# Performance work log

Measured on AMD Instinct MI355X. Metric: run time of the kernel, lower is better.

The kernel has to match this reference:

```python
import jax, jax.numpy as jnp
import numpy as np


def setup_inputs() -> dict:
    key = jax.random.key(0)
    ks = jax.random.split(key, 6)
    B, V, C, T = 32, 2048, 64, 64
    x = jax.random.normal(ks[0], (B, V, C, T), dtype=jnp.float32)
    U_1 = jax.random.normal(ks[1], (V,), dtype=jnp.float32)
    U_2 = jax.random.normal(ks[2], (C, V), dtype=jnp.float32)
    U_3 = jax.random.normal(ks[3], (C,), dtype=jnp.float32)
    b_e = jax.random.normal(ks[4], (1, T, T), dtype=jnp.float32)
    V_e = jax.random.normal(ks[5], (B, T, T), dtype=jnp.float32)
    return {"x": x, "U_1": U_1, "U_2": U_2, "U_3": U_3, "b_e": b_e, "V_e": V_e}


def reference(x, U_1, U_2, U_3, b_e, V_e):
    # x: (B, V, C, T)
    # lhs = (x^T . U_1) . U_2  -> (B, T, V)
    lhs = jnp.einsum('bvct,v->btc', x, U_1) @ U_2          # (B,T,C) @ (C,V) -> (B,T,V)
    # rhs = x^T . U_3 -> (B, V, T)
    rhs = jnp.einsum('bvct,c->bvt', x, U_3)                # (B,V,T)
    product = jnp.einsum('btv,bvu->btu', lhs, rhs)          # (B,T,T)
    # E = V_e @ sigmoid(product + b_e); V_e broadcast over batch
    E = jnp.einsum('bts,bsu->btu', V_e, jax.nn.sigmoid(product + b_e))  # (B,T,T)
    # manual softmax along dim 1 (shift-invariant -> equivalent to jax.nn.softmax)
    return jax.nn.softmax(E, axis=1)
```

## Files before the change

### kernel.cpp

```cpp
#include <hip/hip_runtime.h>
#include <math.h>

#define NB 32
#define NV 2048
#define NC 64
#define NT 64
#define VC 128
#define CHUNKS (NV / VC)
#define U2P 68

__global__ __launch_bounds__(256) void k1_pass_x(
    const float* __restrict__ x,
    const float* __restrict__ U1,
    const float* __restrict__ U2,
    const float* __restrict__ U3,
    float* __restrict__ part)
{
    const int tid = threadIdx.x;
    const int blk = blockIdx.x;
    const int b     = blk / CHUNKS;
    const int chunk = blk % CHUNKS;
    const int v0    = chunk * VC;

    const int w    = tid >> 6;
    const int l    = tid & 63;
    const int u0   = (l & 15) * 4;
    const int crow = l >> 4;
    const int cw   = w * 16 + crow;

    __shared__ float U2s[VC][U2P];
    __shared__ float Msum[NC * NT];

    for (int i = tid; i < VC * NC; i += 256) {
        const int c  = i >> 7;
        const int vi = i & 127;
        U2s[vi][c] = U2[c * NV + v0 + vi];
    }

    float u3r[4];
#pragma unroll
    for (int k = 0; k < 4; ++k) u3r[k] = U3[cw + 4 * k];

    float4 t1r[4], mr[16];
#pragma unroll
    for (int k = 0; k < 4; ++k) t1r[k] = make_float4(0.f, 0.f, 0.f, 0.f);
#pragma unroll
    for (int j = 0; j < 16; ++j) mr[j] = make_float4(0.f, 0.f, 0.f, 0.f);

    __syncthreads();

    const float* xb = x + (size_t)(b * NV + v0) * (NC * NT) + cw * NT + u0;

    float4 xc[4];
#pragma unroll
    for (int k = 0; k < 4; ++k)
        xc[k] = *reinterpret_cast<const float4*>(xb + 4 * k * NT);

#pragma unroll 2
    for (int vi = 0; vi < VC; ++vi) {
        const int vn = (vi + 1 < VC) ? vi + 1 : vi;
        const float* xv = xb + (size_t)vn * (NC * NT);
        float4 xn[4];
#pragma unroll
        for (int k = 0; k < 4; ++k)
            xn[k] = *reinterpret_cast<const float4*>(xv + 4 * k * NT);

        const float u1v = U1[v0 + vi];

        float4 rh = make_float4(0.f, 0.f, 0.f, 0.f);
#pragma unroll
        for (int k = 0; k < 4; ++k) {
            t1r[k].x = fmaf(u1v, xc[k].x, t1r[k].x);
            t1r[k].y = fmaf(u1v, xc[k].y, t1r[k].y);
            t1r[k].z = fmaf(u1v, xc[k].z, t1r[k].z);
            t1r[k].w = fmaf(u1v, xc[k].w, t1r[k].w);
            rh.x = fmaf(u3r[k], xc[k].x, rh.x);
            rh.y = fmaf(u3r[k], xc[k].y, rh.y);
            rh.z = fmaf(u3r[k], xc[k].z, rh.z);
            rh.w = fmaf(u3r[k], xc[k].w, rh.w);
        }

#pragma unroll
        for (int m = 16; m <= 32; m <<= 1) {
            rh.x += __shfl_xor(rh.x, m, 64);
            rh.y += __shfl_xor(rh.y, m, 64);
            rh.z += __shfl_xor(rh.z, m, 64);
            rh.w += __shfl_xor(rh.w, m, 64);
        }

#pragma unroll
        for (int j4 = 0; j4 < 4; ++j4) {
            const float4 u2v = *reinterpret_cast<const float4*>(
                &U2s[vi][crow * 16 + 4 * j4]);
            mr[4 * j4 + 0].x = fmaf(u2v.x, rh.x, mr[4 * j4 + 0].x);
            mr[4 * j4 + 0].y = fmaf(u2v.x, rh.y, mr[4 * j4 + 0].y);
            mr[4 * j4 + 0].z = fmaf(u2v.x, rh.z, mr[4 * j4 + 0].z);
            mr[4 * j4 + 0].w = fmaf(u2v.x, rh.w, mr[4 * j4 + 0].w);
            mr[4 * j4 + 1].x = fmaf(u2v.y, rh.x, mr[4 * j4 + 1].x);
            mr[4 * j4 + 1].y = fmaf(u2v.y, rh.y, mr[4 * j4 + 1].y);
            mr[4 * j4 + 1].z = fmaf(u2v.y, rh.z, mr[4 * j4 + 1].z);
            mr[4 * j4 + 1].w = fmaf(u2v.y, rh.w, mr[4 * j4 + 1].w);
            mr[4 * j4 + 2].x = fmaf(u2v.z, rh.x, mr[4 * j4 + 2].x);
            mr[4 * j4 + 2].y = fmaf(u2v.z, rh.y, mr[4 * j4 + 2].y);
            mr[4 * j4 + 2].z = fmaf(u2v.z, rh.z, mr[4 * j4 + 2].z);
            mr[4 * j4 + 2].w = fmaf(u2v.z, rh.w, mr[4 * j4 + 2].w);
            mr[4 * j4 + 3].x = fmaf(u2v.w, rh.x, mr[4 * j4 + 3].x);
            mr[4 * j4 + 3].y = fmaf(u2v.w, rh.y, mr[4 * j4 + 3].y);
            mr[4 * j4 + 3].z = fmaf(u2v.w, rh.z, mr[4 * j4 + 3].z);
            mr[4 * j4 + 3].w = fmaf(u2v.w, rh.w, mr[4 * j4 + 3].w);
        }

#pragma unroll
        for (int k = 0; k < 4; ++k) xc[k] = xn[k];
    }

    float* pb = part + (size_t)(b * CHUNKS + chunk) * 2 * NC * NT;

#pragma unroll
    for (int k = 0; k < 4; ++k)
        *reinterpret_cast<float4*>(&pb[(cw + 4 * k) * NT + u0]) = t1r[k];

    for (int i = 0; i < 4; ++i) {
        if (w == i) {
#pragma unroll
            for (int j = 0; j < 16; ++j) {
                float* d = &Msum[(crow * 16 + j) * NT + u0];
                if (i == 0) {
                    *reinterpret_cast<float4*>(d) = mr[j];
                } else {
                    d[0] += mr[j].x; d[1] += mr[j].y;
                    d[2] += mr[j].z; d[3] += mr[j].w;
                }
            }
        }
        __syncthreads();
    }

    float* pbM = pb + NC * NT;
    for (int i = tid * 4; i < NC * NT; i += 1024)
        *reinterpret_cast<float4*>(&pbM[i]) =
            *reinterpret_cast<const float4*>(&Msum[i]);
}

__global__ __launch_bounds__(256) void k2a_reduce(
    const float4* __restrict__ part4,
    float4* __restrict__ fin4)
{
    const int j = blockIdx.x;
    const int b = j >> 3;
    const int local = (j & 7) * 256 + threadIdx.x;

    const float4* p = part4 + (size_t)b * CHUNKS * 2048 + local;
    float4 a0 = make_float4(0.f, 0.f, 0.f, 0.f);
    float4 a1 = a0, a2 = a0, a3 = a0;
#pragma unroll
    for (int ch = 0; ch < CHUNKS; ch += 4) {
        const float4 v0 = p[(size_t)(ch + 0) * 2048];
        const float4 v1 = p[(size_t)(ch + 1) * 2048];
        const float4 v2 = p[(size_t)(ch + 2) * 2048];
        const float4 v3 = p[(size_t)(ch + 3) * 2048];
        a0.x += v0.x; a0.y += v0.y; a0.z += v0.z; a0.w += v0.w;
        a1.x += v1.x; a1.y += v1.y; a1.z += v1.z; a1.w += v1.w;
        a2.x += v2.x; a2.y += v2.y; a2.z += v2.z; a2.w += v2.w;
        a3.x += v3.x; a3.y += v3.y; a3.z += v3.z; a3.w += v3.w;
    }
    float4 acc;
    acc.x = (a0.x + a1.x) + (a2.x + a3.x);
    acc.y = (a0.y + a1.y) + (a2.y + a3.y);
    acc.z = (a0.z + a1.z) + (a2.z + a3.z);
    acc.w = (a0.w + a1.w) + (a2.w + a3.w);
    fin4[(size_t)b * 2048 + local] = acc;
}

__global__ __launch_bounds__(256) void k2b_epilogue(
    const float* __restrict__ fin,
    const float* __restrict__ b_e,
    const float* __restrict__ V_e,
    float* __restrict__ out)
{
    const int b = blockIdx.x;
    const int tid = threadIdx.x;

    __shared__ float t1[NC * NT];
    __shared__ float Mb[NC * NT];
    __shared__ float P[NT * NT];
    __shared__ float Eb[NT * NT];

    const float* t1g = fin + (size_t)b * 2 * NC * NT;
    const float* mgb = t1g + NC * NT;
    for (int i = tid * 4; i < NC * NT; i += 1024) {
        *reinterpret_cast<float4*>(&t1[i]) = *reinterpret_cast<const float4*>(&t1g[i]);
        *reinterpret_cast<float4*>(&Mb[i]) = *reinterpret_cast<const float4*>(&mgb[i]);
    }
    __syncthreads();

    const int u  = tid & 63;
    const int tg = tid >> 6;

    for (int i = 0; i < 16; ++i) {
        const int t = tg * 16 + i;
        float acc = 0.f;
#pragma unroll 8
        for (int c = 0; c < NC; ++c)
            acc = fmaf(t1[c * NT + t], Mb[c * NT + u], acc);
        const float z = acc + b_e[t * NT + u];
        P[t * NT + u] = 1.0f / (1.0f + expf(-z));
    }
    __syncthreads();

    const float* veb = V_e + (size_t)b * NT * NT;
    for (int i = 0; i < 16; ++i) {
        const int t = tg * 16 + i;
        float acc = 0.f;
#pragma unroll 8
        for (int s = 0; s < NT; ++s)
            acc = fmaf(veb[t * NT + s], P[s * NT + u], acc);
        Eb[t * NT + u] = acc;
    }
    __syncthreads();

    if (tid < NT) {
        const int uu = tid;
        float m = -INFINITY;
        for (int t = 0; t < NT; ++t) m = fmaxf(m, Eb[t * NT + uu]);
        float ssum = 0.f;
        for (int t = 0; t < NT; ++t) {
            const float e = expf(Eb[t * NT + uu] - m);
            Eb[t * NT + uu] = e;
            ssum += e;
        }
        const float inv = 1.0f / ssum;
        for (int t = 0; t < NT; ++t)
            out[(size_t)b * NT * NT + t * NT + uu] = Eb[t * NT + uu] * inv;
    }
}

extern "C" void kernel_launch(void* const* d_in, const int* in_sizes, int n_in,
                              void* d_out, int out_size, void* d_ws, size_t ws_size,
                              hipStream_t stream) {
    const float* x   = (const float*)d_in[0];
    const float* U1  = (const float*)d_in[1];
    const float* U2  = (const float*)d_in[2];
    const float* U3  = (const float*)d_in[3];
    const float* b_e = (const float*)d_in[4];
    const float* V_e = (const float*)d_in[5];
    float* out = (float*)d_out;

    float* part = (float*)d_ws;
    float* fin  = part + (size_t)NB * CHUNKS * 2 * NC * NT;

    k1_pass_x<<<NB * CHUNKS, 256, 0, stream>>>(x, U1, U2, U3, part);
    k2a_reduce<<<256, 256, 0, stream>>>((const float4*)part, (float4*)fin);
    k2b_epilogue<<<NB, 256, 0, stream>>>(fin, b_e, V_e, out);
}
```

Baseline: 245.4 us.

## Software-pipeline the cross-lane reduction and alias Msum onto U2 shared memory

The k1 main loop is restructured so the butterfly shuffle reduction for iteration vi is interleaved with the rank-1 M accumulation for iteration vi-1. This hides shuffle latency behind independent FMAs, and a peeled epilogue handles the final vector. Msum now reuses the U2 shared buffer, guarded by an added barrier, which lowers LDS use and may allow more blocks per CU. The changes add register pressure from the pipelined state.

```diff
diff --git a/kernel.cpp b/kernel.cpp
--- a/kernel.cpp
+++ b/kernel.cpp
@@ -8,6 +8,8 @@
 #define VC 128
 #define CHUNKS (NV / VC)
 #define U2P 68
+
+typedef float f32x4 __attribute__((ext_vector_type(4)));
 
 __global__ __launch_bounds__(256) void k1_pass_x(
     const float* __restrict__ x,
@@ -28,13 +30,14 @@
     const int crow = l >> 4;
     const int cw   = w * 16 + crow;
 
-    __shared__ float U2s[VC][U2P];
-    __shared__ float Msum[NC * NT];
+    __shared__ float smem[VC * U2P];
+#define U2S(vi, c) smem[(vi) * U2P + (c)]
+    float* Msum = smem;
 
     for (int i = tid; i < VC * NC; i += 256) {
         const int c  = i >> 7;
         const int vi = i & 127;
-        U2s[vi][c] = U2[c * NV + v0 + vi];
+        U2S(vi, c) = U2[c * NV + v0 + vi];
     }
 
     float u3r[4];
@@ -51,67 +54,152 @@
 
     const float* xb = x + (size_t)(b * NV + v0) * (NC * NT) + cw * NT + u0;
 
-    float4 xc[4];
+    f32x4 xc[4];
 #pragma unroll
     for (int k = 0; k < 4; ++k)
-        xc[k] = *reinterpret_cast<const float4*>(xb + 4 * k * NT);
+        xc[k] = *reinterpret_cast<const f32x4*>(xb + 4 * k * NT);
+
+    float4 rh_prev = make_float4(0.f, 0.f, 0.f, 0.f);
 
 #pragma unroll 2
     for (int vi = 0; vi < VC; ++vi) {
         const int vn = (vi + 1 < VC) ? vi + 1 : vi;
         const float* xv = xb + (size_t)vn * (NC * NT);
-        float4 xn[4];
+        f32x4 xn[4];
 #pragma unroll
         for (int k = 0; k < 4; ++k)
-            xn[k] = *reinterpret_cast<const float4*>(xv + 4 * k * NT);
+            xn[k] = *reinterpret_cast<const f32x4*>(xv + 4 * k * NT);
 
         const float u1v = U1[v0 + vi];
 
-        float4 rh = make_float4(0.f, 0.f, 0.f, 0.f);
+        float4 rhn = make_float4(0.f, 0.f, 0.f, 0.f);
 #pragma unroll
         for (int k = 0; k < 4; ++k) {
             t1r[k].x = fmaf(u1v, xc[k].x, t1r[k].x);
             t1r[k].y = fmaf(u1v, xc[k].y, t1r[k].y);
             t1r[k].z = fmaf(u1v, xc[k].z, t1r[k].z);
             t1r[k].w = fmaf(u1v, xc[k].w, t1r[k].w);
-            rh.x = fmaf(u3r[k], xc[k].x, rh.x);
-            rh.y = fmaf(u3r[k], xc[k].y, rh.y);
-            rh.z = fmaf(u3r[k], xc[k].z, rh.z);
-            rh.w = fmaf(u3r[k], xc[k].w, rh.w);
+            rhn.x = fmaf(u3r[k], xc[k].x, rhn.x);
+            rhn.y = fmaf(u3r[k], xc[k].y, rhn.y);
+            rhn.z = fmaf(u3r[k], xc[k].z, rhn.z);
+            rhn.w = fmaf(u3r[k], xc[k].w, rhn.w);
         }
 
-#pragma unroll
-        for (int m = 16; m <= 32; m <<= 1) {
-            rh.x += __shfl_xor(rh.x, m, 64);
-            rh.y += __shfl_xor(rh.y, m, 64);
-            rh.z += __shfl_xor(rh.z, m, 64);
-            rh.w += __shfl_xor(rh.w, m, 64);
-        }
-
+        const float s1x = __shfl_xor(rhn.x, 16, 64);
+        const float s1y = __shfl_xor(rhn.y, 16, 64);
+        const float s1z = __shfl_xor(rhn.z, 16, 64);
+        const float s1w = __shfl_xor(rhn.w, 16, 64);
+
+        const int vp = (vi == 0) ? 0 : vi - 1;
+        const float4 u2a = *reinterpret_cast<const float4*>(&U2S(vp, crow * 16 + 0));
+        const float4 u2b = *reinterpret_cast<const float4*>(&U2S(vp, crow * 16 + 4));
+        mr[0].x = fmaf(u2a.x, rh_prev.x, mr[0].x);
+        mr[0].y = fmaf(u2a.x, rh_prev.y, mr[0].y);
+        mr[0].z = fmaf(u2a.x, rh_prev.z, mr[0].z);
+        mr[0].w = fmaf(u2a.x, rh_prev.w, mr[0].w);
+        mr[1].x = fmaf(u2a.y, rh_prev.x, mr[1].x);
+        mr[1].y = fmaf(u2a.y, rh_prev.y, mr[1].y);
+        mr[1].z = fmaf(u2a.y, rh_prev.z, mr[1].z);
+        mr[1].w = fmaf(u2a.y, rh_prev.w, mr[1].w);
+        mr[2].x = fmaf(u2a.z, rh_prev.x, mr[2].x);
+        mr[2].y = fmaf(u2a.z, rh_prev.y, mr[2].y);
+        mr[2].z = fmaf(u2a.z, rh_prev.z, mr[2].z);
+        mr[2].w = fmaf(u2a.z, rh_prev.w, mr[2].w);
+        mr[3].x = fmaf(u2a.w, rh_prev.x, mr[3].x);
+        mr[3].y = fmaf(u2a.w, rh_prev.y, mr[3].y);
+        mr[3].z = fmaf(u2a.w, rh_prev.z, mr[3].z);
+        mr[3].w = fmaf(u2a.w, rh_prev.w, mr[3].w);
+        mr[4].x = fmaf(u2b.x, rh_prev.x, mr[4].x);
+        mr[4].y = fmaf(u2b.x, rh_prev.y, mr[4].y);
+        mr[4].z = fmaf(u2b.x, rh_prev.z, mr[4].z);
+        mr[4].w = fmaf(u2b.x, rh_prev.w, mr[4].w);
+        mr[5].x = fmaf(u2b.y, rh_prev.x, mr[5].x);
+        mr[5].y = fmaf(u2b.y, rh_prev.y, mr[5].y);
+        mr[5].z = fmaf(u2b.y, rh_prev.z, mr[5].z);
+        mr[5].w = fmaf(u2b.y, rh_prev.w, mr[5].w);
+        mr[6].x = fmaf(u2b.z, rh_prev.x, mr[6].x);
+        mr[6].y = fmaf(u2b.z, rh_prev.y, mr[6].y);
+        mr[6].z = fmaf(u2b.z, rh_prev.z, mr[6].z);
+        mr[6].w = fmaf(u2b.z, rh_prev.w, mr[6].w);
+        mr[7].x = fmaf(u2b.w, rh_prev.x, mr[7].x);
+        mr[7].y = fmaf(u2b.w, rh_prev.y, mr[7].y);
+        mr[7].z = fmaf(u2b.w, rh_prev.z, mr[7].z);
+        mr[7].w = fmaf(u2b.w, rh_prev.w, mr[7].w);
+
+        float cx = rhn.x + s1x, cy = rhn.y + s1y;
+        float cz = rhn.z + s1z, cwv = rhn.w + s1w;
+        const float s2x = __shfl_xor(cx, 32, 64);
+        const float s2y = __shfl_xor(cy, 32, 64);
+        const float s2z = __shfl_xor(cz, 32, 64);
+        const float s2w = __shfl_xor(cwv, 32, 64);
+
+        const float4 u2c = *reinterpret_cast<const float4*>(&U2S(vp, crow * 16 + 8));
+        const float4 u2d = *reinterpret_cast<const float4*>(&U2S(vp, crow * 16 + 12));
+        mr[8].x  = fmaf(u2c.x, rh_prev.x, mr[8].x);
+        mr[8].y  = fmaf(u2c.x, rh_prev.y, mr[8].y);
+        mr[8].z  = fmaf(u2c.x, rh_prev.z, mr[8].z);
+        mr[8].w  = fmaf(u2c.x, rh_prev.w, mr[8].w);
+        mr[9].x  = fmaf(u2c.y, rh_prev.x, mr[9].x);
+        mr[9].y  = fmaf(u2c.y, rh_prev.y, mr[9].y);
+        mr[9].z  = fmaf(u2c.y, rh_prev.z, mr[9].z);
+        mr[9].w  = fmaf(u2c.y, rh_prev.w, mr[9].w);
+        mr[10].x = fmaf(u2c.z, rh_prev.x, mr[10].x);
+        mr[10].y = fmaf(u2c.z, rh_prev.y, mr[10].y);
+        mr[10].z = fmaf(u2c.z, rh_prev.z, mr[10].z);
+        mr[10].w = fmaf(u2c.z, rh_prev.w, mr[10].w);
+        mr[11].x = fmaf(u2c.w, rh_prev.x, mr[11].x);
+        mr[11].y = fmaf(u2c.w, rh_prev.y, mr[11].y);
+        mr[11].z = fmaf(u2c.w, rh_prev.z, mr[11].z);
+        mr[11].w = fmaf(u2c.w, rh_prev.w, mr[11].w);
+        mr[12].x = fmaf(u2d.x, rh_prev.x, mr[12].x);
+        mr[12].y = fmaf(u2d.x, rh_prev.y, mr[12].y);
+        mr[12].z = fmaf(u2d.x, rh_prev.z, mr[12].z);
+        mr[12].w = fmaf(u2d.x, rh_prev.w, mr[12].w);
+        mr[13].x = fmaf(u2d.y, rh_prev.x, mr[13].x);
+        mr[13].y = fmaf(u2d.y, rh_prev.y, mr[13].y);
+        mr[13].z = fmaf(u2d.y, rh_prev.z, mr[13].z);
+        mr[13].w = fmaf(u2d.y, rh_prev.w, mr[13].w);
+        mr[14].x = fmaf(u2d.z, rh_prev.x, mr[14].x);
+        mr[14].y = fmaf(u2d.z, rh_prev.y, mr[14].y);
+        mr[14].z = fmaf(u2d.z, rh_prev.z, mr[14].z);
+        mr[14].w = fmaf(u2d.z, rh_prev.w, mr[14].w);
+        mr[15].x = fmaf(u2d.w, rh_prev.x, mr[15].x);
+        mr[15].y = fmaf(u2d.w, rh_prev.y, mr[15].y);
+        mr[15].z = fmaf(u2d.w, rh_prev.z, mr[15].z);
+        mr[15].w = fmaf(u2d.w, rh_prev.w, mr[15].w);
+
+        rh_prev.x = cx + s2x;
+        rh_prev.y = cy + s2y;
+        rh_prev.z = cz + s2z;
+        rh_prev.w = cwv + s2w;
+
+#pragma unroll
+        for (int k = 0; k < 4; ++k) xc[k] = xn[k];
+    }
+
+    {
+        const int vp = VC - 1;
 #pragma unroll
         for (int j4 = 0; j4 < 4; ++j4) {
             const float4 u2v = *reinterpret_cast<const float4*>(
-                &U2s[vi][crow * 16 + 4 * j4]);
-            mr[4 * j4 + 0].x = fmaf(u2v.x, rh.x, mr[4 * j4 + 0].x);
-            mr[4 * j4 + 0].y = fmaf(u2v.x, rh.y, mr[4 * j4 + 0].y);
-            mr[4 * j4 + 0].z = fmaf(u2v.x, rh.z, mr[4 * j4 + 0].z);
-            mr[4 * j4 + 0].w = fmaf(u2v.x, rh.w, mr[4 * j4 + 0].w);
-            mr[4 * j4 + 1].x = fmaf(u2v.y, rh.x, mr[4 * j4 + 1].x);
-            mr[4 * j4 + 1].y = fmaf(u2v.y, rh.y, mr[4 * j4 + 1].y);
-            mr[4 * j4 + 1].z = fmaf(u2v.y, rh.z, mr[4 * j4 + 1].z);
-            mr[4 * j4 + 1].w = fmaf(u2v.y, rh.w, mr[4 * j4 + 1].w);
-            mr[4 * j4 + 2].x = fmaf(u2v.z, rh.x, mr[4 * j4 + 2].x);
-            mr[4 * j4 + 2].y = fmaf(u2v.z, rh.y, mr[4 * j4 + 2].y);
-            mr[4 * j4 + 2].z = fmaf(u2v.z, rh.z, mr[4 * j4 + 2].z);
-            mr[4 * j4 + 2].w = fmaf(u2v.z, rh.w, mr[4 * j4 + 2].w);
-            mr[4 * j4 + 3].x = fmaf(u2v.w, rh.x, mr[4 * j4 + 3].x);
-            mr[4 * j4 + 3].y = fmaf(u2v.w, rh.y, mr[4 * j4 + 3].y);
-            mr[4 * j4 + 3].z = fmaf(u2v.w, rh.z, mr[4 * j4 + 3].z);
-            mr[4 * j4 + 3].w = fmaf(u2v.w, rh.w, mr[4 * j4 + 3].w);
+                &U2S(vp, crow * 16 + 4 * j4));
+            mr[4 * j4 + 0].x = fmaf(u2v.x, rh_prev.x, mr[4 * j4 + 0].x);
+            mr[4 * j4 + 0].y = fmaf(u2v.x, rh_prev.y, mr[4 * j4 + 0].y);
+            mr[4 * j4 + 0].z = fmaf(u2v.x, rh_prev.z, mr[4 * j4 + 0].z);
+            mr[4 * j4 + 0].w = fmaf(u2v.x, rh_prev.w, mr[4 * j4 + 0].w);
+            mr[4 * j4 + 1].x = fmaf(u2v.y, rh_prev.x, mr[4 * j4 + 1].x);
+            mr[4 * j4 + 1].y = fmaf(u2v.y, rh_prev.y, mr[4 * j4 + 1].y);
+            mr[4 * j4 + 1].z = fmaf(u2v.y, rh_prev.z, mr[4 * j4 + 1].z);
+            mr[4 * j4 + 1].w = fmaf(u2v.y, rh_prev.w, mr[4 * j4 + 1].w);
+            mr[4 * j4 + 2].x = fmaf(u2v.z, rh_prev.x, mr[4 * j4 + 2].x);
+            mr[4 * j4 + 2].y = fmaf(u2v.z, rh_prev.y, mr[4 * j4 + 2].y);
+            mr[4 * j4 + 2].z = fmaf(u2v.z, rh_prev.z, mr[4 * j4 + 2].z);
+            mr[4 * j4 + 2].w = fmaf(u2v.z, rh_prev.w, mr[4 * j4 + 2].w);
+            mr[4 * j4 + 3].x = fmaf(u2v.w, rh_prev.x, mr[4 * j4 + 3].x);
+            mr[4 * j4 + 3].y = fmaf(u2v.w, rh_prev.y, mr[4 * j4 + 3].y);
+            mr[4 * j4 + 3].z = fmaf(u2v.w, rh_prev.z, mr[4 * j4 + 3].z);
+            mr[4 * j4 + 3].w = fmaf(u2v.w, rh_prev.w, mr[4 * j4 + 3].w);
         }
-
-#pragma unroll
-        for (int k = 0; k < 4; ++k) xc[k] = xn[k];
     }
 
     float* pb = part + (size_t)(b * CHUNKS + chunk) * 2 * NC * NT;
@@ -119,6 +207,8 @@
 #pragma unroll
     for (int k = 0; k < 4; ++k)
         *reinterpret_cast<float4*>(&pb[(cw + 4 * k) * NT + u0]) = t1r[k];
+
+    __syncthreads();
 
     for (int i = 0; i < 4; ++i) {
         if (w == i) {
```

Result: no change. 248.6 us (+1.3%).
